# Optimization experiments

Measured on AMD Instinct MI355X. Metric: run time of the kernel, lower is better.

The kernel has to match this reference:

```python
import jax, jax.numpy as jnp
import numpy as np
from jax import lax

B, N, S, K, C = 8, 4096, 1024, 64, 64
RADIUS = 0.2
MLP = [64, 128, 256]
INT_MAX = jnp.iinfo(jnp.int32).max

_batched_gather = jax.vmap(lambda a, i: a[i])  # (N,D),(S,K)->(S,K,D)


def setup_inputs() -> dict:
    key = jax.random.key(0)
    ks = jax.random.split(key, 6)
    xyz = jax.random.uniform(ks[0], (B, N, 3), dtype=jnp.float32)
    points = jax.random.normal(ks[1], (B, N, C), dtype=jnp.float32)
    fps_inds = jax.random.randint(ks[2], (B, S), 0, N, dtype=jnp.int32)
    c_in = [3 + C] + MLP[:-1]
    w0 = jax.random.normal(ks[3], (c_in[0], MLP[0]), dtype=jnp.float32) * 0.1
    w1 = jax.random.normal(ks[4], (c_in[1], MLP[1]), dtype=jnp.float32) * 0.1
    w2 = jax.random.normal(ks[5], (c_in[2], MLP[2]), dtype=jnp.float32) * 0.1
    return {"xyz": xyz, "points": points, "fps_inds": fps_inds,
            "w0": w0, "w1": w1, "w2": w2}


def _query_ball_point(radius, nsample, xyz, new_xyz):
    # dists: (B, S, N)
    dists = jnp.linalg.norm(new_xyz[:, :, None, :] - xyz[:, None, :, :], axis=-1)
    # nsample nearest neighbors (ascending distance), like argsort[:, :, :nsample]
    neg_d, idx = lax.top_k(-dists, nsample)            # (B,S,K)
    valid = (-neg_d) < radius                          # prefix mask (dists ascending)
    idx_m = jnp.where(valid, idx, INT_MAX)
    sidx = jnp.sort(idx_m, axis=-1)
    # invalid slots -> first (smallest) valid index
    return jnp.where(valid, sidx, sidx[:, :, :1])


def reference(xyz, points, fps_inds, w0, w1, w2):
    new_xyz = _batched_gather(xyz, fps_inds)                       # (B,S,3)
    idx = _query_ball_point(RADIUS, K, xyz, new_xyz)               # (B,S,K)
    grouped_xyz = _batched_gather(xyz, idx) - new_xyz[:, :, None]  # (B,S,K,3)
    grouped_pts = _batched_gather(points, idx)                     # (B,S,K,C)
    feat = jnp.concatenate([grouped_xyz, grouped_pts], axis=-1)    # (B,S,K,3+C)
    for w in (w0, w1, w2):  # 1x1 conv == channel matmul, then relu
        feat = jax.nn.relu(jnp.einsum('bskc,cf->bskf', feat, w))
    new_points = jnp.max(feat, axis=2)                             # (B,S,F)
    return new_xyz, new_points
```

## Files before the change

kernel.cpp:

```cpp
#include <hip/hip_runtime.h>

#define NB 8
#define NN 4096
#define NS 1024
#define NC 64
#define OUT_PTS_OFF (NB*NS*3)
#define CAP2 256
#define RB 0.2f
#define QPB 4

typedef __attribute__((ext_vector_type(8))) short bf16x8;
typedef __attribute__((ext_vector_type(4))) float f32x4;
typedef unsigned long long u64;

static __device__ __forceinline__ short f2bf(float f){
  unsigned u = __float_as_uint(f);
  unsigned r = (u + 0x7FFFu + ((u>>16)&1u)) >> 16;
  return (short)r;
}
static __device__ __forceinline__ float bf2f(short s){
  return __uint_as_float(((unsigned)(unsigned short)s) << 16);
}
static __device__ __forceinline__ unsigned cvtpk(float a, float b){
  unsigned r;
  asm("v_cvt_pk_bf16_f32 %0, %1, %2" : "=v"(r) : "v"(a), "v"(b));
  return r;
}

#define WS_PX1_SH   1048576
#define WS_WF_SH    3145728

__global__ __launch_bounds__(256) void prep_grid(
    const float* __restrict__ w0, const float* __restrict__ w1,
    const float* __restrict__ w2, short* __restrict__ ws,
    const float* __restrict__ xyz, float4* __restrict__ gxyz,
    int* __restrict__ cstart)
{
  __shared__ int hist[125];
  __shared__ int base[125];
  const int tid = threadIdx.x;

  if (blockIdx.x < 184) {
    int e = blockIdx.x*256 + tid;
    if (e >= 47104) return;
    float v = 0.f;
    if (e < 6144) {
      int j=e&7, l=(e>>3)&63, nt=(e>>9)&3, kt=e>>11;
      int k = kt*32 + ((l>>4)<<3) + j, n = nt*16 + (l&15);
      if (k < 64) v = w0[(3+k)*64 + n];
      else if (k < 67) v = w0[(k-64)*64 + n];
    } else if (e < 14336) {
      int e2=e-6144;
      int j=e2&7, l=(e2>>3)&63, nt=(e2>>9)&7, kt=e2>>12;
      int k = kt*32 + ((l>>4)<<3) + j, n = nt*16 + (l&15);
      v = w1[k*128 + n];
    } else {
      int e3=e-14336;
      int j=e3&7, l=(e3>>3)&63, nt=(e3>>9)&15, kt=e3>>13;
      int k = (kt*2 + (j&1))*16 + ((l>>4)<<2) + (j>>1);
      v = w2[k*256 + nt*16 + (l&15)];
    }
    ws[e] = f2bf(v);
    return;
  }

  const int b = blockIdx.x - 184;
  const float* xb = xyz + (size_t)b*NN*3;
  if (tid < 125) hist[tid] = 0;
  __syncthreads();

  float xs[16], ys[16], zs[16]; int cl[16];
  {
    const float4* xv = (const float4*)(xb + tid*48);
    #pragma unroll
    for (int g=0; g<4; ++g) {
      float4 v0 = xv[g*3], v1 = xv[g*3+1], v2 = xv[g*3+2];
      xs[g*4+0]=v0.x; xs[g*4+1]=v0.w; xs[g*4+2]=v1.z; xs[g*4+3]=v2.y;
      ys[g*4+0]=v0.y; ys[g*4+1]=v1.x; ys[g*4+2]=v1.w; ys[g*4+3]=v2.z;
      zs[g*4+0]=v0.z; zs[g*4+1]=v1.y; zs[g*4+2]=v2.x; zs[g*4+3]=v2.w;
    }
  }
  #pragma unroll
  for (int r=0; r<16; ++r) {
    int cx = min(4, (int)(xs[r]*5.0f));
    int cy = min(4, (int)(ys[r]*5.0f));
    int cz = min(4, (int)(zs[r]*5.0f));
    cl[r] = (cz*5+cy)*5+cx;
    atomicAdd(&hist[cl[r]], 1);
  }
  __syncthreads();
  if (tid == 0) {
    int acc = 0;
    for (int c=0; c<125; ++c) { base[c]=acc; cstart[b*128+c]=acc; acc+=hist[c]; }
    cstart[b*128+125] = NN;
  }
  __syncthreads();
  #pragma unroll
  for (int r=0; r<16; ++r) {
    int slot = atomicAdd(&base[cl[r]], 1);
    gxyz[b*NN + slot] = make_float4(xs[r], ys[r], zs[r], __int_as_float(tid*16+r));
  }
}

__global__ __launch_bounds__(256) void px1_select(
    const float* __restrict__ xyz, const float* __restrict__ points,
    const int* __restrict__ fps_inds, const short* __restrict__ wsb,
    const float4* __restrict__ gxyz, const int* __restrict__ cstart,
    short* __restrict__ px1, unsigned short* __restrict__ gsidx,
    float* __restrict__ out)
{
  __shared__ u64 candk[4][CAP2];
  __shared__ int tmpi[4][64];
  __shared__ int segS[4][28], segB[4][28], segE[4][28];
  __shared__ int scell[126];

  const int tid = threadIdx.x;

  if (blockIdx.x < 512) {
    const int w = tid>>6, l = tid&63, lr = l&15, grp = l>>4;
    const int rowbase = blockIdx.x*64 + w*16;
    const int row = rowbase + lr;
    const float* prow = points + (size_t)row*NC;
    const float* xr   = xyz + (size_t)row*3;

    bf16x8 a0, a1, a2;
    {
      float4 u0 = *(const float4*)(prow + grp*8);
      float4 u1 = *(const float4*)(prow + grp*8 + 4);
      float4 u2 = *(const float4*)(prow + 32 + grp*8);
      float4 u3 = *(const float4*)(prow + 32 + grp*8 + 4);
      a0 = (bf16x8){f2bf(u0.x),f2bf(u0.y),f2bf(u0.z),f2bf(u0.w),f2bf(u1.x),f2bf(u1.y),f2bf(u1.z),f2bf(u1.w)};
      a1 = (bf16x8){f2bf(u2.x),f2bf(u2.y),f2bf(u2.z),f2bf(u2.w),f2bf(u3.x),f2bf(u3.y),f2bf(u3.z),f2bf(u3.w)};
      short e0=0,e1=0,e2v=0;
      if (grp==0) { e0=f2bf(xr[0]); e1=f2bf(xr[1]); e2v=f2bf(xr[2]); }
      a2 = (bf16x8){e0,e1,e2v,0,0,0,0,0};
    }
    f32x4 zero4 = {0.f,0.f,0.f,0.f};
    #pragma unroll
    for (int nt=0; nt<4; ++nt) {
      f32x4 acc = zero4;
      bf16x8 b0 = *(const bf16x8*)(wsb + (((0*4+nt)*64 + l)<<3));
      bf16x8 b1 = *(const bf16x8*)(wsb + (((1*4+nt)*64 + l)<<3));
      bf16x8 b2 = *(const bf16x8*)(wsb + (((2*4+nt)*64 + l)<<3));
      acc = __builtin_amdgcn_mfma_f32_16x16x32_bf16(a0, b0, acc, 0,0,0);
      acc = __builtin_amdgcn_mfma_f32_16x16x32_bf16(a1, b1, acc, 0,0,0);
      acc = __builtin_amdgcn_mfma_f32_16x16x32_bf16(a2, b2, acc, 0,0,0);
      #pragma unroll
      for (int i=0;i<4;++i)
        px1[(size_t)(rowbase + grp*4 + i)*64 + nt*16 + lr] = f2bf(acc[i]);
    }
    return;
  }

  const int sb = blockIdx.x - 512;
  const int wv = tid>>6, lane = tid&63;
  const int q = sb*QPB + wv, b = q >> 10;
  const float* xb = xyz + (size_t)b*NN*3;

  if (tid < 126) scell[tid] = cstart[b*128+tid];
  __syncthreads();

  const int fps = fps_inds[q];
  const float qx = xb[fps*3+0], qy = xb[fps*3+1], qz = xb[fps*3+2];
  if (lane < 3) out[q*3+lane] = xb[fps*3+lane];

  int len = 0, s = 0;
  if (lane < 27) {
    const int cx = min(4, (int)(qx*5.0f));
    const int cy = min(4, (int)(qy*5.0f));
    const int cz = min(4, (int)(qz*5.0f));
    int ncx = cx + lane%3 - 1, ncy = cy + (lane/3)%3 - 1, ncz = cz + lane/9 - 1;
    if (ncx>=0 && ncx<5 && ncy>=0 && ncy<5 && ncz>=0 && ncz<5) {
      float lox = ncx*0.2f - 1e-5f, hix = lox + 0.2f + 2e-5f;
      float loy = ncy*0.2f - 1e-5f, hiy = loy + 0.2f + 2e-5f;
      float loz = ncz*0.2f - 1e-5f, hiz = loz + 0.2f + 2e-5f;
      float dx = fmaxf(0.f, fmaxf(lox-qx, qx-hix));
      float dy = fmaxf(0.f, fmaxf(loy-qy, qy-hiy));
      float dz = fmaxf(0.f, fmaxf(loz-qz, qz-hiz));
      if (fmaf(dx,dx, fmaf(dy,dy, dz*dz)) <= 0.0402f) {
        int c = (ncz*5+ncy)*5+ncx;
        s = scell[c]; len = scell[c+1] - s;
      }
    }
  }
  int incl = len;
  #pragma unroll
  for (int off=1; off<64; off<<=1) {
    int v = __shfl_up(incl, off, 64);
    if (lane >= off) incl += v;
  }
  const int T = __shfl(incl, 26, 64);
  if (lane < 27) { segS[wv][lane]=s; segB[wv][lane]=incl-len; segE[wv][lane]=incl; }
  __builtin_amdgcn_wave_barrier();

  const float4* gb = gxyz + b*NN;
  int base = 0, k = 0;
  const int rounds = (T + 63) >> 6;
  const u64 ltmask = (1ull << lane) - 1ull;
  for (int r = 0; r < rounds; ++r) {
    int t = r*64 + lane;
    bool hit = false; u64 key = 0;
    if (t < T) {
      while (t >= segE[wv][k]) ++k;
      float4 p = gb[segS[wv][k] + (t - segB[wv][k])];
      float fx = qx-p.x, fy = qy-p.y, fz = qz-p.z;
      float ff = fmaf(fx,fx, fmaf(fy,fy, fz*fz));
      if (ff < 0.0402f) {
        float dx=__fsub_rn(qx,p.x), dy=__fsub_rn(qy,p.y), dz=__fsub_rn(qz,p.z);
        float d2=__fadd_rn(__fadd_rn(__fmul_rn(dx,dx),__fmul_rn(dy,dy)),__fmul_rn(dz,dz));
        float d = __fsqrt_rn(d2);
        if (d < RB) {
          hit = true;
          key = ((u64)__float_as_uint(d) << 16) | (u64)(unsigned)__float_as_int(p.w);
        }
      }
    }
    u64 m = __ballot(hit);
    int pos = base + (int)__popcll(m & ltmask);
    if (hit && pos < CAP2) candk[wv][pos] = key;
    base += (int)__popcll(m);
  }
  int cnt = base < CAP2 ? base : CAP2;
  __builtin_amdgcn_wave_barrier();

  if (cnt > 64) {
    for (int j = lane; j < cnt; j += 64) {
      u64 kj = candk[wv][j];
      int rk = 0;
      for (int i = 0; i < cnt; ++i) rk += (int)(candk[wv][i] < kj);
      if (rk < 64) tmpi[wv][rk] = (int)(kj & 0xFFFFu);
    }
    __builtin_amdgcn_wave_barrier();
    int v = tmpi[wv][lane];
    int p = 0;
    #pragma unroll 8
    for (int u = 0; u < 64; ++u) p += (int)(tmpi[wv][u] < v);
    gsidx[q*64 + p] = (unsigned short)v;
  } else {
    if (lane < cnt) {
      int v = (int)(candk[wv][lane] & 0xFFFFu);
      int p = 0;
      for (int u = 0; u < cnt; ++u) p += (int)((int)(candk[wv][u] & 0xFFFFu) < v);
      tmpi[wv][p] = v;
    }
    __builtin_amdgcn_wave_barrier();
    gsidx[q*64 + lane] = (unsigned short)tmpi[wv][lane < cnt ? lane : 0];
  }
}

__global__ __launch_bounds__(256,2) void mlp_kernel(
    const float* __restrict__ xyz, const int* __restrict__ fps_inds,
    const float* __restrict__ w0, const short* __restrict__ wsb,
    const short* __restrict__ px1, const unsigned short* __restrict__ gsidx,
    float* __restrict__ out)
{
  __shared__ __align__(16) short h2f[2][8192];
  __shared__ float q1s[QPB][64];
  __shared__ int sidx[QPB][64];

  const int tid = threadIdx.x;
  const int w = tid>>6, l = tid&63, lr = l&15, grp = l>>4;
  const int q0 = blockIdx.x*QPB;
  const int b = q0 >> 10;
  const float* xb = xyz + (size_t)b*NN*3;

  bf16x8 b3[4][4];
  #pragma unroll
  for (int kt=0; kt<4; ++kt)
    #pragma unroll
    for (int j=0; j<4; ++j)
      b3[kt][j] = *(const bf16x8*)(wsb + 14336 + (((kt*16 + w*4 + j)*64 + l)<<3));

  {
    int qq = tid>>6, t = tid&63;
    int fp = fps_inds[q0+qq];
    sidx[qq][t] = (int)gsidx[(q0+qq)*64 + t];
    q1s[qq][t] = xb[fp*3]*w0[t] + xb[fp*3+1]*w0[64+t] + xb[fp*3+2]*w0[128+t];
  }
  if (tid < QPB*3) {
    int qq = tid/3, c = tid - qq*3;
    int fp = fps_inds[q0+qq];
    out[(q0+qq)*3 + c] = xb[fp*3+c];
  }
  __syncthreads();

  const short* px1b = px1 + (size_t)b*NN*64;
  const short* w1g  = wsb + 6144;
  const int myrow = w*16 + lr;

  f32x4 zero4 = {0.f,0.f,0.f,0.f};
  const int uu4 = (lr>>2) << 4;
  const int gg4 = grp << 4;

  auto MKA = [&](int qq, const bf16x8& v0, const bf16x8& v1, bf16x8& a20, bf16x8& a21) {
    union { unsigned u[4]; bf16x8 v; } ua, ub;
    #pragma unroll
    for (int jp=0; jp<4; ++jp) {
      float x0 = fmaxf(bf2f(v0[2*jp  ]) - q1s[qq][grp*8+2*jp  ], 0.f);
      float x1 = fmaxf(bf2f(v0[2*jp+1]) - q1s[qq][grp*8+2*jp+1], 0.f);
      ua.u[jp] = cvtpk(x0, x1);
      float y0 = fmaxf(bf2f(v1[2*jp  ]) - q1s[qq][32+grp*8+2*jp  ], 0.f);
      float y1 = fmaxf(bf2f(v1[2*jp+1]) - q1s[qq][32+grp*8+2*jp+1], 0.f);
      ub.u[jp] = cvtpk(y0, y1);
    }
    a20 = ua.v; a21 = ub.v;
  };

  auto LAYER2 = [&](const bf16x8& a20, const bf16x8& a21, int p) {
    char* hb = (char*)h2f + p*16384;
    #pragma unroll
    for (int ntp=0; ntp<4; ++ntp) {
      f32x4 accA = zero4, accB = zero4;
      bf16x8 bA0 = *(const bf16x8*)(w1g + (((0*8 + 2*ntp  )*64 + l)<<3));
      bf16x8 bA1 = *(const bf16x8*)(w1g + (((1*8 + 2*ntp  )*64 + l)<<3));
      bf16x8 bB0 = *(const bf16x8*)(w1g + (((0*8 + 2*ntp+1)*64 + l)<<3));
      bf16x8 bB1 = *(const bf16x8*)(w1g + (((1*8 + 2*ntp+1)*64 + l)<<3));
      accA = __builtin_amdgcn_mfma_f32_16x16x32_bf16(a20, bA0, accA, 0,0,0);
      accA = __builtin_amdgcn_mfma_f32_16x16x32_bf16(a21, bA1, accA, 0,0,0);
      accB = __builtin_amdgcn_mfma_f32_16x16x32_bf16(a20, bB0, accB, 0,0,0);
      accB = __builtin_amdgcn_mfma_f32_16x16x32_bf16(a21, bB1, accB, 0,0,0);
      #pragma unroll
      for (int i=0; i<4; ++i) {
        unsigned pv = cvtpk(fmaxf(accA[i],0.f), fmaxf(accB[i],0.f));
        int byteoff = ((((w*4+ntp)*64 + (lr>>2)*16 + grp*4 + i)<<4) + ((lr&3)<<2)) ^ uu4;
        *(unsigned*)(hb + byteoff) = pv;
      }
    }
  };

  bf16x8 v0, v1, a20, a21;
  {
    int idx = sidx[0][myrow];
    v0 = *(const bf16x8*)(px1b + idx*64 + grp*8);
    v1 = *(const bf16x8*)(px1b + idx*64 + 32 + grp*8);
  }
  MKA(0, v0, v1, a20, a21);
  {
    int idx = sidx[1][myrow];
    v0 = *(const bf16x8*)(px1b + idx*64 + grp*8);
    v1 = *(const bf16x8*)(px1b + idx*64 + 32 + grp*8);
  }
  LAYER2(a20, a21, 0);
  __syncthreads();

  #pragma unroll
  for (int qq = 0; qq < QPB; ++qq) {
    const int cur = qq & 1;

    if (qq+1 < QPB) {
      MKA(qq+1, v0, v1, a20, a21);
      if (qq+2 < QPB) {
        int idx = sidx[qq+2][myrow];
        v0 = *(const bf16x8*)(px1b + idx*64 + grp*8);
        v1 = *(const bf16x8*)(px1b + idx*64 + 32 + grp*8);
      }
      LAYER2(a20, a21, cur^1);
    }

    const char* hb = (const char*)h2f + cur*16384;
    float rm[4][4];
    #pragma unroll
    for (int j=0;j<4;++j)
      #pragma unroll
      for (int i=0;i<4;++i) rm[j][i] = 0.f;
    #pragma unroll
    for (int mt=0; mt<4; ++mt) {
      f32x4 acc[4] = {zero4, zero4, zero4, zero4};
      #pragma unroll
      for (int kt=0; kt<4; ++kt) {
        int byteoff = ((((mt*4+kt)*64 + l)<<4)) ^ gg4;
        bf16x8 a = *(const bf16x8*)(hb + byteoff);
        #pragma unroll
        for (int j=0; j<4; ++j)
          acc[j] = __builtin_amdgcn_mfma_f32_16x16x32_bf16(a, b3[kt][j], acc[j], 0,0,0);
      }
      #pragma unroll
      for (int j=0; j<4; ++j)
        #pragma unroll
        for (int i=0; i<4; ++i) rm[j][i] = fmaxf(rm[j][i], acc[j][i]);
    }
    #pragma unroll
    for (int j=0; j<4; ++j) {
      float m = fmaxf(fmaxf(rm[j][0],rm[j][1]), fmaxf(rm[j][2],rm[j][3]));
      m = fmaxf(m, __shfl_xor(m, 16, 64));
      m = fmaxf(m, __shfl_xor(m, 32, 64));
      if (grp == 0) out[OUT_PTS_OFF + (q0+qq)*256 + (w*4+j)*16 + lr] = m;
    }

    if (qq+1 < QPB) __syncthreads();
  }
}

extern "C" void kernel_launch(void* const* d_in, const int* in_sizes, int n_in,
                              void* d_out, int out_size, void* d_ws, size_t ws_size,
                              hipStream_t stream) {
  const float* xyz      = (const float*)d_in[0];
  const float* points   = (const float*)d_in[1];
  const int*   fps_inds = (const int*)d_in[2];
  const float* w0       = (const float*)d_in[3];
  const float* w1       = (const float*)d_in[4];
  const float* w2       = (const float*)d_in[5];
  float* out = (float*)d_out;

  unsigned short* gsidx = (unsigned short*)d_ws;
  float4* gxyz  = (float4*)((char*)d_ws + 1048576);
  int*    cstart= (int*)((char*)d_ws + 1572864);
  short*  px1   = (short*)d_ws + WS_PX1_SH;
  short*  wsb   = (short*)d_ws + WS_WF_SH;

  hipLaunchKernelGGL(prep_grid,  dim3(192), dim3(256), 0, stream,
                     w0, w1, w2, wsb, xyz, gxyz, cstart);
  hipLaunchKernelGGL(px1_select, dim3(512 + NB*NS/QPB), dim3(256), 0, stream,
                     xyz, points, fps_inds, wsb, gxyz, cstart, px1, gsidx, out);
  hipLaunchKernelGGL(mlp_kernel, dim3(NB*NS/QPB), dim3(256), 0, stream,
                     xyz, fps_inds, w0, wsb, px1, gsidx, out);
}
```

Baseline: 97.04 us.

## Warp-specialize MLP kernel into producer and consumer waves with register-resident weights

Doubles the MLP block to 512 threads. Waves 0-3 act as producers: they gather features, apply layer 1 and compute layer 2 into a shared double buffer. Waves 4-7 act as consumers: they compute layer 3 and the max reduction. Producers now keep the layer-2 weights in registers instead of reloading them from global memory for every query. The two stages are meant to run concurrently, at the cost of more waves per block, possibly lower occupancy under the launch bound, and producer and consumer work that may be imbalanced.

```diff
diff --git a/kernel.cpp b/kernel.cpp
--- a/kernel.cpp
+++ b/kernel.cpp
@@ -248,7 +248,7 @@
   }
 }
 
-__global__ __launch_bounds__(256,2) void mlp_kernel(
+__global__ __launch_bounds__(512,2) void mlp_kernel(
     const float* __restrict__ xyz, const int* __restrict__ fps_inds,
     const float* __restrict__ w0, const short* __restrict__ wsb,
     const short* __restrict__ px1, const unsigned short* __restrict__ gsidx,
@@ -259,19 +259,31 @@
   __shared__ int sidx[QPB][64];
 
   const int tid = threadIdx.x;
-  const int w = tid>>6, l = tid&63, lr = l&15, grp = l>>4;
+  const int wv = tid>>6, l = tid&63, lr = l&15, grp = l>>4;
+  const bool isProd = (wv < 4);
+  const int w = isProd ? wv : (wv - 4);
   const int q0 = blockIdx.x*QPB;
   const int b = q0 >> 10;
   const float* xb = xyz + (size_t)b*NN*3;
 
-  bf16x8 b3[4][4];
-  #pragma unroll
-  for (int kt=0; kt<4; ++kt)
-    #pragma unroll
-    for (int j=0; j<4; ++j)
-      b3[kt][j] = *(const bf16x8*)(wsb + 14336 + (((kt*16 + w*4 + j)*64 + l)<<3));
-
-  {
+  bf16x8 wreg[4][4];
+  if (isProd) {
+    #pragma unroll
+    for (int ntp=0; ntp<4; ++ntp) {
+      wreg[ntp][0] = *(const bf16x8*)(wsb + 6144 + (((0*8 + 2*ntp  )*64 + l)<<3));
+      wreg[ntp][1] = *(const bf16x8*)(wsb + 6144 + (((1*8 + 2*ntp  )*64 + l)<<3));
+      wreg[ntp][2] = *(const bf16x8*)(wsb + 6144 + (((0*8 + 2*ntp+1)*64 + l)<<3));
+      wreg[ntp][3] = *(const bf16x8*)(wsb + 6144 + (((1*8 + 2*ntp+1)*64 + l)<<3));
+    }
+  } else {
+    #pragma unroll
+    for (int kt=0; kt<4; ++kt)
+      #pragma unroll
+      for (int j=0; j<4; ++j)
+        wreg[kt][j] = *(const bf16x8*)(wsb + 14336 + (((kt*16 + w*4 + j)*64 + l)<<3));
+  }
+
+  if (tid < QPB*64) {
     int qq = tid>>6, t = tid&63;
     int fp = fps_inds[q0+qq];
     sidx[qq][t] = (int)gsidx[(q0+qq)*64 + t];
@@ -285,7 +297,6 @@
   __syncthreads();
 
   const short* px1b = px1 + (size_t)b*NN*64;
-  const short* w1g  = wsb + 6144;
   const int myrow = w*16 + lr;
 
   f32x4 zero4 = {0.f,0.f,0.f,0.f};
@@ -311,14 +322,10 @@
     #pragma unroll
     for (int ntp=0; ntp<4; ++ntp) {
       f32x4 accA = zero4, accB = zero4;
-      bf16x8 bA0 = *(const bf16x8*)(w1g + (((0*8 + 2*ntp  )*64 + l)<<3));
-      bf16x8 bA1 = *(const bf16x8*)(w1g + (((1*8 + 2*ntp  )*64 + l)<<3));
-      bf16x8 bB0 = *(const bf16x8*)(w1g + (((0*8 + 2*ntp+1)*64 + l)<<3));
-      bf16x8 bB1 = *(const bf16x8*)(w1g + (((1*8 + 2*ntp+1)*64 + l)<<3));
-      accA = __builtin_amdgcn_mfma_f32_16x16x32_bf16(a20, bA0, accA, 0,0,0);
-      accA = __builtin_amdgcn_mfma_f32_16x16x32_bf16(a21, bA1, accA, 0,0,0);
-      accB = __builtin_amdgcn_mfma_f32_16x16x32_bf16(a20, bB0, accB, 0,0,0);
-      accB = __builtin_amdgcn_mfma_f32_16x16x32_bf16(a21, bB1, accB, 0,0,0);
+      accA = __builtin_amdgcn_mfma_f32_16x16x32_bf16(a20, wreg[ntp][0], accA, 0,0,0);
+      accA = __builtin_amdgcn_mfma_f32_16x16x32_bf16(a21, wreg[ntp][1], accA, 0,0,0);
+      accB = __builtin_amdgcn_mfma_f32_16x16x32_bf16(a20, wreg[ntp][2], accB, 0,0,0);
+      accB = __builtin_amdgcn_mfma_f32_16x16x32_bf16(a21, wreg[ntp][3], accB, 0,0,0);
       #pragma unroll
       for (int i=0; i<4; ++i) {
         unsigned pv = cvtpk(fmaxf(accA[i],0.f), fmaxf(accB[i],0.f));
@@ -329,64 +336,61 @@
   };
 
   bf16x8 v0, v1, a20, a21;
-  {
+  if (isProd) {
     int idx = sidx[0][myrow];
     v0 = *(const bf16x8*)(px1b + idx*64 + grp*8);
     v1 = *(const bf16x8*)(px1b + idx*64 + 32 + grp*8);
-  }
-  MKA(0, v0, v1, a20, a21);
-  {
-    int idx = sidx[1][myrow];
-    v0 = *(const bf16x8*)(px1b + idx*64 + grp*8);
-    v1 = *(const bf16x8*)(px1b + idx*64 + 32 + grp*8);
-  }
-  LAYER2(a20, a21, 0);
+    MKA(0, v0, v1, a20, a21);
+    int idx1 = sidx[1][myrow];
+    v0 = *(const bf16x8*)(px1b + idx1*64 + grp*8);
+    v1 = *(const bf16x8*)(px1b + idx1*64 + 32 + grp*8);
+    LAYER2(a20, a21, 0);
+  }
   __syncthreads();
 
   #pragma unroll
   for (int qq = 0; qq < QPB; ++qq) {
-    const int cur = qq & 1;
-
-    if (qq+1 < QPB) {
-      MKA(qq+1, v0, v1, a20, a21);
-      if (qq+2 < QPB) {
-        int idx = sidx[qq+2][myrow];
-        v0 = *(const bf16x8*)(px1b + idx*64 + grp*8);
-        v1 = *(const bf16x8*)(px1b + idx*64 + 32 + grp*8);
-      }
-      LAYER2(a20, a21, cur^1);
-    }
-
-    const char* hb = (const char*)h2f + cur*16384;
-    float rm[4][4];
-    #pragma unroll
-    for (int j=0;j<4;++j)
-      #pragma unroll
-      for (int i=0;i<4;++i) rm[j][i] = 0.f;
-    #pragma unroll
-    for (int mt=0; mt<4; ++mt) {
-      f32x4 acc[4] = {zero4, zero4, zero4, zero4};
-      #pragma unroll
-      for (int kt=0; kt<4; ++kt) {
-        int byteoff = ((((mt*4+kt)*64 + l)<<4)) ^ gg4;
-        bf16x8 a = *(const bf16x8*)(hb + byteoff);
+    if (isProd) {
+      if (qq+1 < QPB) {
+        MKA(qq+1, v0, v1, a20, a21);
+        if (qq+2 < QPB) {
+          int idx = sidx[qq+2][myrow];
+          v0 = *(const bf16x8*)(px1b + idx*64 + grp*8);
+          v1 = *(const bf16x8*)(px1b + idx*64 + 32 + grp*8);
+        }
+        LAYER2(a20, a21, (qq+1)&1);
+      }
+    } else {
+      const char* hb = (const char*)h2f + (qq&1)*16384;
+      float rm[4][4];
+      #pragma unroll
+      for (int j=0;j<4;++j)
+        #pragma unroll
+        for (int i=0;i<4;++i) rm[j][i] = 0.f;
+      #pragma unroll
+      for (int mt=0; mt<4; ++mt) {
+        f32x4 acc[4] = {zero4, zero4, zero4, zero4};
+        #pragma unroll
+        for (int kt=0; kt<4; ++kt) {
+          int byteoff = ((((mt*4+kt)*64 + l)<<4)) ^ gg4;
+          bf16x8 a = *(const bf16x8*)(hb + byteoff);
+          #pragma unroll
+          for (int j=0; j<4; ++j)
+            acc[j] = __builtin_amdgcn_mfma_f32_16x16x32_bf16(a, wreg[kt][j], acc[j], 0,0,0);
+        }
         #pragma unroll
         for (int j=0; j<4; ++j)
-          acc[j] = __builtin_amdgcn_mfma_f32_16x16x32_bf16(a, b3[kt][j], acc[j], 0,0,0);
-      }
-      #pragma unroll
-      for (int j=0; j<4; ++j)
-        #pragma unroll
-        for (int i=0; i<4; ++i) rm[j][i] = fmaxf(rm[j][i], acc[j][i]);
-    }
-    #pragma unroll
-    for (int j=0; j<4; ++j) {
-      float m = fmaxf(fmaxf(rm[j][0],rm[j][1]), fmaxf(rm[j][2],rm[j][3]));
-      m = fmaxf(m, __shfl_xor(m, 16, 64));
-      m = fmaxf(m, __shfl_xor(m, 32, 64));
-      if (grp == 0) out[OUT_PTS_OFF + (q0+qq)*256 + (w*4+j)*16 + lr] = m;
-    }
-
+          #pragma unroll
+          for (int i=0; i<4; ++i) rm[j][i] = fmaxf(rm[j][i], acc[j][i]);
+      }
+      #pragma unroll
+      for (int j=0; j<4; ++j) {
+        float m = fmaxf(fmaxf(rm[j][0],rm[j][1]), fmaxf(rm[j][2],rm[j][3]));
+        m = fmaxf(m, __shfl_xor(m, 16, 64));
+        m = fmaxf(m, __shfl_xor(m, 32, 64));
+        if (grp == 0) out[OUT_PTS_OFF + (q0+qq)*256 + (w*4+j)*16 + lr] = m;
+      }
+    }
     if (qq+1 < QPB) __syncthreads();
   }
 }
@@ -412,6 +416,6 @@
                      w0, w1, w2, wsb, xyz, gxyz, cstart);
   hipLaunchKernelGGL(px1_select, dim3(512 + NB*NS/QPB), dim3(256), 0, stream,
                      xyz, points, fps_inds, wsb, gxyz, cstart, px1, gsidx, out);
-  hipLaunchKernelGGL(mlp_kernel, dim3(NB*NS/QPB), dim3(256), 0, stream,
+  hipLaunchKernelGGL(mlp_kernel, dim3(NB*NS/QPB), dim3(512), 0, stream,
                      xyz, fps_inds, w0, wsb, px1, gsidx, out);
 }
```

Result: slower. 109.0 us (+12.3%).
